# Optimization experiments

Measured on AMD Instinct MI355X. Metric: run time of the kernel, lower is better.

Reference implementation:

```python
import jax, jax.numpy as jnp
import numpy as np

EMBED_DIM = 768
NUM_HEADS = 12
HEAD_DIM = EMBED_DIM // NUM_HEADS
SCALE = HEAD_DIM ** -0.5


def setup_inputs() -> dict:
    key = jax.random.key(0)
    k_x, k_wqkv, k_bqkv, k_wp, k_bp = jax.random.split(key, 5)
    B, N, D = 16, 1024, EMBED_DIM
    x = jax.random.normal(k_x, (B, N, D), dtype=jnp.float32)
    # nn.Linear default init: U(-1/sqrt(fan_in), 1/sqrt(fan_in))
    bound = 1.0 / np.sqrt(D)
    W_qkv = jax.random.uniform(k_wqkv, (D, 3 * D), minval=-bound, maxval=bound, dtype=jnp.float32)
    b_qkv = jax.random.uniform(k_bqkv, (3 * D,), minval=-bound, maxval=bound, dtype=jnp.float32)
    W_proj = jax.random.uniform(k_wp, (D, D), minval=-bound, maxval=bound, dtype=jnp.float32)
    b_proj = jax.random.uniform(k_bp, (D,), minval=-bound, maxval=bound, dtype=jnp.float32)
    return {"x": x, "W_qkv": W_qkv, "b_qkv": b_qkv, "W_proj": W_proj, "b_proj": b_proj}


def reference(x, W_qkv, b_qkv, W_proj, b_proj):
    B, N, D = x.shape
    H, Hd = NUM_HEADS, HEAD_DIM
    qkv = x @ W_qkv + b_qkv                      # [B, N, 3D]
    qkv = qkv.reshape(B, N, 3, H, Hd)
    qkv = jnp.transpose(qkv, (2, 0, 3, 1, 4))    # [3, B, H, N, Hd]
    q, k, v = qkv[0], qkv[1], qkv[2]
    attn = jnp.einsum('bhnd,bhmd->bhnm', q, k) * SCALE  # [B, H, N, N]
    attn = jax.nn.softmax(attn, axis=-1)
    out = jnp.einsum('bhnm,bhmd->bhnd', attn, v)        # [B, H, N, Hd]
    out = jnp.transpose(out, (0, 2, 1, 3)).reshape(B, N, D)
    return out @ W_proj + b_proj
```

## Files before the change

### kernel.cpp

```cpp
#include <hip/hip_runtime.h>
#include <math.h>

typedef _Float16 f16;
typedef _Float16 f16x8 __attribute__((ext_vector_type(8)));
typedef _Float16 f16x4 __attribute__((ext_vector_type(4)));
typedef float    f32x4 __attribute__((ext_vector_type(4)));

#define AS1 __attribute__((address_space(1)))
#define AS3 __attribute__((address_space(3)))

__device__ __forceinline__ void gload16(const void* g, void* l) {
    __builtin_amdgcn_global_load_lds((const AS1 void*)g, (AS3 void*)l, 16, 0, 0);
}

__global__ __launch_bounds__(256) void cast_x_k(const float* __restrict__ in,
                                                f16* __restrict__ out, int n8)
{
    int i = blockIdx.x * 256 + threadIdx.x;
    const int stride = gridDim.x * 256;
    const float4* in4 = (const float4*)in;
    f16x8* o8 = (f16x8*)out;
    for (; i < n8; i += stride) {
        float4 a = in4[2 * i], b = in4[2 * i + 1];
        f16x8 o = {(f16)a.x, (f16)a.y, (f16)a.z, (f16)a.w,
                   (f16)b.x, (f16)b.y, (f16)b.z, (f16)b.w};
        o8[i] = o;
    }
}

__global__ __launch_bounds__(256) void castT_k(const float* __restrict__ W,
                                               f16* __restrict__ WT, int K, int N)
{
    __shared__ float tile[32][33];
    const int k0 = blockIdx.y * 32, n0 = blockIdx.x * 32;
    const int t = threadIdx.x;
    const int r = t >> 3, cq = t & 7;
    float4 v = *(const float4*)&W[(size_t)(k0 + r) * N + n0 + cq * 4];
    tile[r][cq * 4 + 0] = v.x; tile[r][cq * 4 + 1] = v.y;
    tile[r][cq * 4 + 2] = v.z; tile[r][cq * 4 + 3] = v.w;
    __syncthreads();
    f16x4 pk = {(f16)tile[cq * 4 + 0][r], (f16)tile[cq * 4 + 1][r],
                (f16)tile[cq * 4 + 2][r], (f16)tile[cq * 4 + 3][r]};
    *(f16x4*)&WT[(size_t)(n0 + r) * K + k0 + cq * 4] = pk;
}

__global__ __launch_bounds__(256) void vtrans_k(const f16* __restrict__ V,
                                                f16* __restrict__ VT)
{
    __shared__ __align__(16) f16 tile[64][72];
    const int bh = blockIdx.y, tt = blockIdx.x;
    const int t = threadIdx.x;
    const size_t base = (size_t)bh * 1024 * 64;
    {
        int tok = t >> 2, d0 = (t & 3) * 16;
        const f16* src = V + base + (size_t)(tt * 64 + tok) * 64 + d0;
        *(f16x8*)&tile[tok][d0]     = *(const f16x8*)src;
        *(f16x8*)&tile[tok][d0 + 8] = *(const f16x8*)(src + 8);
    }
    __syncthreads();
    {
        int d = t >> 2, ck = t & 3;
        f16 tmp[16];
#pragma unroll
        for (int j = 0; j < 16; ++j) tmp[j] = tile[ck * 16 + j][d];
        f16* dst = VT + base + (size_t)d * 1024 + tt * 64 + ck * 16;
        *(f16x8*)dst       = *(f16x8*)&tmp[0];
        *(f16x8*)(dst + 8) = *(f16x8*)&tmp[8];
    }
}

#define GEMM_MAIN(APTR, BTPTR)                                                   \
    __shared__ __align__(16) f16 As[128 * 64];                                   \
    __shared__ __align__(16) f16 Bs[128 * 64];                                   \
    const int t = threadIdx.x, lid = t & 63, wid = t >> 6;                       \
    const int wr = wid >> 1, wc = wid & 1;                                       \
    const int bm = blockIdx.y, bn = blockIdx.x;                                  \
    f32x4 acc[4][4] = {};                                                        \
    const int srow8 = lid >> 3;                                                  \
    const int sc = (lid & 7) ^ srow8;                                            \
    const f16* aG = (APTR) + (size_t)(bm * 128 + wid * 32 + srow8) * 768 + sc * 8;\
    const f16* bG = (BTPTR) + (size_t)(bn * 128 + wid * 32 + srow8) * 768 + sc * 8;\
    f16* ldsA = As + wid * 32 * 64;                                              \
    f16* ldsB = Bs + wid * 32 * 64;                                              \
    for (int k0 = 0; k0 < 768; k0 += 64) {                                       \
        __syncthreads();                                                         \
        _Pragma("unroll")                                                        \
        for (int c = 0; c < 4; ++c) {                                            \
            gload16(aG + c * 8 * 768 + k0, ldsA + c * 8 * 64);                   \
            gload16(bG + c * 8 * 768 + k0, ldsB + c * 8 * 64);                   \
        }                                                                        \
        __syncthreads();                                                         \
        _Pragma("unroll")                                                        \
        for (int kh = 0; kh < 2; ++kh) {                                         \
            f16x8 af[4], bf[4];                                                  \
            _Pragma("unroll")                                                    \
            for (int m = 0; m < 4; ++m) {                                        \
                int row = wr * 64 + m * 16 + (lid & 15);                         \
                int slot = (kh * 4 + (lid >> 4)) ^ (row & 7);                    \
                af[m] = *(const f16x8*)&As[row * 64 + slot * 8];                 \
                int col = wc * 64 + m * 16 + (lid & 15);                         \
                int slotb = (kh * 4 + (lid >> 4)) ^ (col & 7);                   \
                bf[m] = *(const f16x8*)&Bs[col * 64 + slotb * 8];                \
            }                                                                    \
            _Pragma("unroll")                                                    \
            for (int m = 0; m < 4; ++m)                                          \
                _Pragma("unroll")                                                \
                for (int n = 0; n < 4; ++n)                                      \
                    acc[m][n] = __builtin_amdgcn_mfma_f32_16x16x32_f16(          \
                        af[m], bf[n], acc[m][n], 0, 0, 0);                       \
        }                                                                        \
    }

__global__ __launch_bounds__(256)
void qkv_gemm16(const f16* __restrict__ A, const f16* __restrict__ BT,
                const float* __restrict__ bias,
                f16* __restrict__ qws, f16* __restrict__ kws, f16* __restrict__ vws)
{
    GEMM_MAIN(A, BT)
    const int g = lid >> 4, cl = lid & 15;
#pragma unroll
    for (int m = 0; m < 4; ++m) {
        int rbase = bm * 128 + wr * 64 + m * 16 + g * 4;
#pragma unroll
        for (int n = 0; n < 4; ++n) {
            int cg = bn * 128 + wc * 64 + n * 16 + cl;
            float bb = bias[cg];
            int which = cg / 768;
            int rem = cg - which * 768;
            int h = rem >> 6, d = rem & 63;
            f16* dst = (which == 0) ? qws : (which == 1) ? kws : vws;
            float scl = (which == 0) ? 0.125f : 1.0f;
#pragma unroll
            for (int r = 0; r < 4; ++r) {
                int row = rbase + r;
                int b = row >> 10, tok = row & 1023;
                dst[((size_t)(b * 12 + h) * 1024 + tok) * 64 + d] =
                    (f16)((acc[m][n][r] + bb) * scl);
            }
        }
    }
}

__global__ __launch_bounds__(256)
void proj_gemm16(const f16* __restrict__ A, const f16* __restrict__ BT,
                 const float* __restrict__ bias, float* __restrict__ C)
{
    GEMM_MAIN(A, BT)
    const int g = lid >> 4, cl = lid & 15;
#pragma unroll
    for (int m = 0; m < 4; ++m) {
        int rbase = bm * 128 + wr * 64 + m * 16 + g * 4;
#pragma unroll
        for (int n = 0; n < 4; ++n) {
            int cg = bn * 128 + wc * 64 + n * 16 + cl;
            float bb = bias[cg];
#pragma unroll
            for (int r = 0; r < 4; ++r)
                C[(size_t)(rbase + r) * 768 + cg] = acc[m][n][r] + bb;
        }
    }
}

__global__ __launch_bounds__(256)
void attn16(const f16* __restrict__ Q, const f16* __restrict__ K,
            const f16* __restrict__ VT, f16* __restrict__ AO)
{
    __shared__ __align__(16) f16 kbuf[2][64 * 64];
    __shared__ __align__(16) f16 vbuf[2][64 * 64];
    __shared__ __align__(16) f16 plds[4][16 * 64];

    const int t = threadIdx.x, lid = t & 63, wid = t >> 6;
    const int phys = blockIdx.y * gridDim.x + blockIdx.x;
    const int logical = (phys & 7) * 384 + (phys >> 3);
    const int bh = logical >> 4, qt = logical & 15;

    const int g = lid >> 4, c = lid & 15;
    const size_t hb = (size_t)bh * (1024 * 64);
    const int q0 = qt * 64 + wid * 16;

    const f16* qrow = Q + hb + (size_t)(q0 + c) * 64;
    const f16x8 qf0 = *(const f16x8*)(qrow + g * 8);
    const f16x8 qf1 = *(const f16x8*)(qrow + 32 + g * 8);

    const int srow   = wid * 16 + (lid >> 3);
    const int schunk = ((lid & 7) ^ (lid >> 3)) * 8;

#define ATTN_STAGE(BUF, KT)                                                      \
    {                                                                            \
        const f16* kb_ = K + hb + (size_t)((KT) * 64) * 64;                      \
        const f16* vb_ = VT + hb + (KT) * 64;                                    \
        _Pragma("unroll")                                                        \
        for (int c2 = 0; c2 < 2; ++c2) {                                         \
            gload16(kb_ + (size_t)(srow + c2 * 8) * 64 + schunk,                 \
                    &kbuf[BUF][wid * 1024 + c2 * 512]);                          \
            gload16(vb_ + (size_t)(srow + c2 * 8) * 1024 + schunk,               \
                    &vbuf[BUF][wid * 1024 + c2 * 512]);                          \
        }                                                                        \
    }

    f32x4 o[4] = {};
    float mrun = -INFINITY, lrun = 0.f;
    f16* myp = &plds[wid][0];

    ATTN_STAGE(0, 0)
    __syncthreads();

    int cur = 0;
    for (int kt = 0; kt < 16; ++kt) {
        if (kt < 15) ATTN_STAGE(cur ^ 1, kt + 1)

        const f16* kcur = &kbuf[cur][0];
        const f16* vcur = &vbuf[cur][0];
        const int sw = c & 7;

        f32x4 s[4] = {};
#pragma unroll
        for (int m = 0; m < 4; ++m) {
            const int row = m * 16 + c;
            f16x8 k0f = *(const f16x8*)&kcur[row * 64 + ((g) ^ sw) * 8];
            f16x8 k1f = *(const f16x8*)&kcur[row * 64 + ((4 + g) ^ sw) * 8];
            s[m] = __builtin_amdgcn_mfma_f32_16x16x32_f16(k0f, qf0, s[m], 0, 0, 0);
            s[m] = __builtin_amdgcn_mfma_f32_16x16x32_f16(k1f, qf1, s[m], 0, 0, 0);
        }
        float tmax = s[0][0];
#pragma unroll
        for (int m = 0; m < 4; ++m)
#pragma unroll
            for (int r = 0; r < 4; ++r) tmax = fmaxf(tmax, s[m][r]);
        tmax = fmaxf(tmax, __shfl_xor(tmax, 16));
        tmax = fmaxf(tmax, __shfl_xor(tmax, 32));
        float mnew = fmaxf(mrun, tmax);
        float al = __expf(mrun - mnew);
        float ps = 0.f;
        float pe[4][4];
#pragma unroll
        for (int m = 0; m < 4; ++m)
#pragma unroll
            for (int r = 0; r < 4; ++r) {
                float p = __expf(s[m][r] - mnew);
                pe[m][r] = p; ps += p;
            }
        ps += __shfl_xor(ps, 16);
        ps += __shfl_xor(ps, 32);
        lrun = lrun * al + ps;
        mrun = mnew;
#pragma unroll
        for (int m = 0; m < 4; ++m) {
            f16x4 pk = {(f16)pe[m][0], (f16)pe[m][1], (f16)pe[m][2], (f16)pe[m][3]};
            int slot = (2 * m + (g >> 1)) ^ sw;
            *(f16x4*)&myp[c * 64 + slot * 8 + (g & 1) * 4] = pk;
        }
        float al4[4];
#pragma unroll
        for (int r = 0; r < 4; ++r) al4[r] = __shfl(al, g * 4 + r);
#pragma unroll
        for (int n = 0; n < 4; ++n) {
            o[n][0] *= al4[0]; o[n][1] *= al4[1];
            o[n][2] *= al4[2]; o[n][3] *= al4[3];
        }
        f16x8 pa[2];
#pragma unroll
        for (int kh = 0; kh < 2; ++kh) {
            int slot = (kh * 4 + g) ^ sw;
            pa[kh] = *(const f16x8*)&myp[c * 64 + slot * 8];
        }
#pragma unroll
        for (int kh = 0; kh < 2; ++kh)
#pragma unroll
            for (int n = 0; n < 4; ++n) {
                const int row = n * 16 + c;
                f16x8 vf = *(const f16x8*)&vcur[row * 64 + ((kh * 4 + g) ^ sw) * 8];
                o[n] = __builtin_amdgcn_mfma_f32_16x16x32_f16(pa[kh], vf, o[n], 0, 0, 0);
            }

        __syncthreads();
        cur ^= 1;
    }

    float il = 1.0f / lrun;
    float il4[4];
#pragma unroll
    for (int r = 0; r < 4; ++r) il4[r] = __shfl(il, g * 4 + r);
    const int b = bh / 12, h = bh - b * 12;
#pragma unroll
    for (int n = 0; n < 4; ++n)
#pragma unroll
        for (int r = 0; r < 4; ++r) {
            int tok = q0 + g * 4 + r;
            AO[(size_t)(b * 1024 + tok) * 768 + h * 64 + n * 16 + c] =
                (f16)(o[n][r] * il4[r]);
        }
}


extern "C" void kernel_launch(void* const* d_in, const int* in_sizes, int n_in,
                              void* d_out, int out_size, void* d_ws, size_t ws_size,
                              hipStream_t stream)
{
    const float* x      = (const float*)d_in[0];
    const float* W_qkv  = (const float*)d_in[1];
    const float* b_qkv  = (const float*)d_in[2];
    const float* W_proj = (const float*)d_in[3];
    const float* b_proj = (const float*)d_in[4];
    float* out = (float*)d_out;

    const size_t per = (size_t)16 * 1024 * 768;
    f16* x16    = (f16*)d_ws;
    f16* wqkvT  = x16 + per;
    f16* wprojT = wqkvT + (size_t)768 * 2304;
    f16* qws    = wprojT + (size_t)768 * 768;
    f16* kws    = qws + per;
    f16* vws    = kws + per;
    f16* vt     = vws + per;
    f16* aws    = vt + per;

    cast_x_k<<<3072, 256, 0, stream>>>(x, x16, (int)(per / 8));
    castT_k<<<dim3(2304 / 32, 768 / 32), 256, 0, stream>>>(W_qkv, wqkvT, 768, 2304);
    castT_k<<<dim3(768 / 32, 768 / 32), 256, 0, stream>>>(W_proj, wprojT, 768, 768);
    qkv_gemm16<<<dim3(18, 128), 256, 0, stream>>>(x16, wqkvT, b_qkv, qws, kws, vws);
    vtrans_k<<<dim3(16, 192), 256, 0, stream>>>(vws, vt);
    attn16<<<dim3(16, 192), 256, 0, stream>>>(qws, kws, vt, aws);
    proj_gemm16<<<dim3(6, 128), 256, 0, stream>>>(aws, wprojT, b_proj, out);
}
```

Before: 341.9 us.

## Pipeline GEMMs with 4-stage LDS ring, fuse V transpose, add lazy softmax rescale

The two GEMMs now use 256x256 tiles with 512 threads, a 4-deep global-to-LDS prefetch ring in 32-wide K slices, XCD-aware block remapping and setprio around the MFMA blocks. The QKV epilogue writes V already transposed, which removes the separate vtrans kernel. Attention folds log2(e) into the Q scale so it can use exp2. It also skips rescaling the output accumulator when the running max grows by no more than a threshold. The trade-offs are higher register and LDS pressure in the GEMMs and a risk of f16 overflow in P if the threshold logic is wrong.

```diff
diff --git a/kernel.cpp b/kernel.cpp
--- a/kernel.cpp
+++ b/kernel.cpp
@@ -8,6 +8,8 @@
 
 #define AS1 __attribute__((address_space(1)))
 #define AS3 __attribute__((address_space(3)))
+
+#define QSCALE 0.1803368800f
 
 __device__ __forceinline__ void gload16(const void* g, void* l) {
     __builtin_amdgcn_global_load_lds((const AS1 void*)g, (AS3 void*)l, 16, 0, 0);
@@ -44,115 +46,111 @@
     *(f16x4*)&WT[(size_t)(n0 + r) * K + k0 + cq * 4] = pk;
 }
 
-__global__ __launch_bounds__(256) void vtrans_k(const f16* __restrict__ V,
-                                                f16* __restrict__ VT)
-{
-    __shared__ __align__(16) f16 tile[64][72];
-    const int bh = blockIdx.y, tt = blockIdx.x;
-    const int t = threadIdx.x;
-    const size_t base = (size_t)bh * 1024 * 64;
-    {
-        int tok = t >> 2, d0 = (t & 3) * 16;
-        const f16* src = V + base + (size_t)(tt * 64 + tok) * 64 + d0;
-        *(f16x8*)&tile[tok][d0]     = *(const f16x8*)src;
-        *(f16x8*)&tile[tok][d0 + 8] = *(const f16x8*)(src + 8);
-    }
-    __syncthreads();
-    {
-        int d = t >> 2, ck = t & 3;
-        f16 tmp[16];
-#pragma unroll
-        for (int j = 0; j < 16; ++j) tmp[j] = tile[ck * 16 + j][d];
-        f16* dst = VT + base + (size_t)d * 1024 + tt * 64 + ck * 16;
-        *(f16x8*)dst       = *(f16x8*)&tmp[0];
-        *(f16x8*)(dst + 8) = *(f16x8*)&tmp[8];
-    }
-}
-
-#define GEMM_MAIN(APTR, BTPTR)                                                   \
-    __shared__ __align__(16) f16 As[128 * 64];                                   \
-    __shared__ __align__(16) f16 Bs[128 * 64];                                   \
+#define GEMM_PIPE(APTR, BTPTR, NBN, PERX)                                        \
+    __shared__ __align__(16) f16 As[4][256 * 32];                                \
+    __shared__ __align__(16) f16 Bs[4][256 * 32];                                \
     const int t = threadIdx.x, lid = t & 63, wid = t >> 6;                       \
-    const int wr = wid >> 1, wc = wid & 1;                                       \
-    const int bm = blockIdx.y, bn = blockIdx.x;                                  \
-    f32x4 acc[4][4] = {};                                                        \
-    const int srow8 = lid >> 3;                                                  \
-    const int sc = (lid & 7) ^ srow8;                                            \
-    const f16* aG = (APTR) + (size_t)(bm * 128 + wid * 32 + srow8) * 768 + sc * 8;\
-    const f16* bG = (BTPTR) + (size_t)(bn * 128 + wid * 32 + srow8) * 768 + sc * 8;\
-    f16* ldsA = As + wid * 32 * 64;                                              \
-    f16* ldsB = Bs + wid * 32 * 64;                                              \
-    for (int k0 = 0; k0 < 768; k0 += 64) {                                       \
-        __syncthreads();                                                         \
-        _Pragma("unroll")                                                        \
-        for (int c = 0; c < 4; ++c) {                                            \
-            gload16(aG + c * 8 * 768 + k0, ldsA + c * 8 * 64);                   \
-            gload16(bG + c * 8 * 768 + k0, ldsB + c * 8 * 64);                   \
+    const int wr = wid >> 2, wc = wid & 3;                                       \
+    const int g = lid >> 4, cl = lid & 15;                                       \
+    const int flat = blockIdx.x;                                                 \
+    const int logical = (flat & 7) * (PERX) + (flat >> 3);                       \
+    const int bm = logical / (NBN), bn = logical % (NBN);                        \
+    f32x4 acc[8][4] = {};                                                        \
+    const f16* aG[2]; const f16* bG[2]; int ldsoff[2];                           \
+    _Pragma("unroll")                                                            \
+    for (int i = 0; i < 2; ++i) {                                                \
+        int c_lin = wid * 128 + i * 64 + lid;                                    \
+        int row = c_lin >> 2, ch = c_lin & 3;                                    \
+        int sch = ch ^ (row & 3);                                                \
+        aG[i] = (APTR) + (size_t)(bm * 256 + row) * 768 + sch * 8;               \
+        bG[i] = (BTPTR) + (size_t)(bn * 256 + row) * 768 + sch * 8;              \
+        ldsoff[i] = (wid * 128 + i * 64) * 8;                                    \
+    }                                                                            \
+    _Pragma("unroll")                                                            \
+    for (int p = 0; p < 3; ++p) {                                                \
+        _Pragma("unroll")                                                        \
+        for (int i = 0; i < 2; ++i) {                                            \
+            gload16(aG[i] + p * 32, &As[p][ldsoff[i]]);                          \
+            gload16(bG[i] + p * 32, &Bs[p][ldsoff[i]]);                          \
         }                                                                        \
-        __syncthreads();                                                         \
-        _Pragma("unroll")                                                        \
-        for (int kh = 0; kh < 2; ++kh) {                                         \
-            f16x8 af[4], bf[4];                                                  \
+    }                                                                            \
+    for (int kt = 0; kt < 24; ++kt) {                                            \
+        int tn = kt + 3; if (tn >= 24) tn -= 24;    \
+        _Pragma("unroll")                                                        \
+        for (int i = 0; i < 2; ++i) {                                            \
+            gload16(aG[i] + tn * 32, &As[tn & 3][ldsoff[i]]);                    \
+            gload16(bG[i] + tn * 32, &Bs[tn & 3][ldsoff[i]]);                    \
+        }                                                                        \
+        asm volatile("s_waitcnt vmcnt(12)" ::: "memory");                        \
+        __builtin_amdgcn_s_barrier();                                            \
+        const f16* As_ = &As[kt & 3][0];                                         \
+        const f16* Bs_ = &Bs[kt & 3][0];                                         \
+        const int slotx = (g ^ (cl & 3)) * 8;                                    \
+        f16x8 af[8], bf[4];                                                      \
+        _Pragma("unroll")                                                        \
+        for (int m = 0; m < 8; ++m)                                              \
+            af[m] = *(const f16x8*)&As_[(wr * 128 + m * 16 + cl) * 32 + slotx];  \
+        _Pragma("unroll")                                                        \
+        for (int n = 0; n < 4; ++n)                                              \
+            bf[n] = *(const f16x8*)&Bs_[(wc * 64 + n * 16 + cl) * 32 + slotx];   \
+        __builtin_amdgcn_s_setprio(1);                                           \
+        _Pragma("unroll")                                                        \
+        for (int m = 0; m < 8; ++m)                                              \
             _Pragma("unroll")                                                    \
-            for (int m = 0; m < 4; ++m) {                                        \
-                int row = wr * 64 + m * 16 + (lid & 15);                         \
-                int slot = (kh * 4 + (lid >> 4)) ^ (row & 7);                    \
-                af[m] = *(const f16x8*)&As[row * 64 + slot * 8];                 \
-                int col = wc * 64 + m * 16 + (lid & 15);                         \
-                int slotb = (kh * 4 + (lid >> 4)) ^ (col & 7);                   \
-                bf[m] = *(const f16x8*)&Bs[col * 64 + slotb * 8];                \
-            }                                                                    \
-            _Pragma("unroll")                                                    \
-            for (int m = 0; m < 4; ++m)                                          \
-                _Pragma("unroll")                                                \
-                for (int n = 0; n < 4; ++n)                                      \
-                    acc[m][n] = __builtin_amdgcn_mfma_f32_16x16x32_f16(          \
-                        af[m], bf[n], acc[m][n], 0, 0, 0);                       \
-        }                                                                        \
-    }
-
-__global__ __launch_bounds__(256)
+            for (int n = 0; n < 4; ++n)                                          \
+                acc[m][n] = __builtin_amdgcn_mfma_f32_16x16x32_f16(              \
+                    af[m], bf[n], acc[m][n], 0, 0, 0);                           \
+        __builtin_amdgcn_s_setprio(0);                                           \
+        __builtin_amdgcn_s_barrier();                                            \
+    }
+
+__global__ __launch_bounds__(512, 2)
 void qkv_gemm16(const f16* __restrict__ A, const f16* __restrict__ BT,
                 const float* __restrict__ bias,
-                f16* __restrict__ qws, f16* __restrict__ kws, f16* __restrict__ vws)
-{
-    GEMM_MAIN(A, BT)
-    const int g = lid >> 4, cl = lid & 15;
-#pragma unroll
-    for (int m = 0; m < 4; ++m) {
-        int rbase = bm * 128 + wr * 64 + m * 16 + g * 4;
+                f16* __restrict__ qws, f16* __restrict__ kws, f16* __restrict__ vt)
+{
+    GEMM_PIPE(A, BT, 9, 72)
+#pragma unroll
+    for (int m = 0; m < 8; ++m) {
+        int rbase = bm * 256 + wr * 128 + m * 16 + g * 4;
 #pragma unroll
         for (int n = 0; n < 4; ++n) {
-            int cg = bn * 128 + wc * 64 + n * 16 + cl;
+            int cg = bn * 256 + wc * 64 + n * 16 + cl;
             float bb = bias[cg];
             int which = cg / 768;
             int rem = cg - which * 768;
             int h = rem >> 6, d = rem & 63;
-            f16* dst = (which == 0) ? qws : (which == 1) ? kws : vws;
-            float scl = (which == 0) ? 0.125f : 1.0f;
-#pragma unroll
-            for (int r = 0; r < 4; ++r) {
-                int row = rbase + r;
-                int b = row >> 10, tok = row & 1023;
-                dst[((size_t)(b * 12 + h) * 1024 + tok) * 64 + d] =
-                    (f16)((acc[m][n][r] + bb) * scl);
+            if (which == 2) {
+                int b = rbase >> 10, tok = rbase & 1023;
+                f16x4 pk = {(f16)(acc[m][n][0] + bb), (f16)(acc[m][n][1] + bb),
+                            (f16)(acc[m][n][2] + bb), (f16)(acc[m][n][3] + bb)};
+                *(f16x4*)&vt[((size_t)(b * 12 + h) * 64 + d) * 1024 + tok] = pk;
+            } else {
+                f16* dst = which ? kws : qws;
+                float scl = which ? 1.0f : QSCALE;
+#pragma unroll
+                for (int r = 0; r < 4; ++r) {
+                    int row = rbase + r;
+                    int b = row >> 10, tok = row & 1023;
+                    dst[((size_t)(b * 12 + h) * 1024 + tok) * 64 + d] =
+                        (f16)((acc[m][n][r] + bb) * scl);
+                }
             }
         }
     }
 }
 
-__global__ __launch_bounds__(256)
+__global__ __launch_bounds__(512, 2)
 void proj_gemm16(const f16* __restrict__ A, const f16* __restrict__ BT,
                  const float* __restrict__ bias, float* __restrict__ C)
 {
-    GEMM_MAIN(A, BT)
-    const int g = lid >> 4, cl = lid & 15;
-#pragma unroll
-    for (int m = 0; m < 4; ++m) {
-        int rbase = bm * 128 + wr * 64 + m * 16 + g * 4;
+    GEMM_PIPE(A, BT, 3, 24)
+#pragma unroll
+    for (int m = 0; m < 8; ++m) {
+        int rbase = bm * 256 + wr * 128 + m * 16 + g * 4;
 #pragma unroll
         for (int n = 0; n < 4; ++n) {
-            int cg = bn * 128 + wc * 64 + n * 16 + cl;
+            int cg = bn * 256 + wc * 64 + n * 16 + cl;
             float bb = bias[cg];
 #pragma unroll
             for (int r = 0; r < 4; ++r)
@@ -214,6 +212,7 @@
         const int sw = c & 7;
 
         f32x4 s[4] = {};
+        __builtin_amdgcn_s_setprio(1);
 #pragma unroll
         for (int m = 0; m < 4; ++m) {
             const int row = m * 16 + c;
@@ -222,48 +221,61 @@
             s[m] = __builtin_amdgcn_mfma_f32_16x16x32_f16(k0f, qf0, s[m], 0, 0, 0);
             s[m] = __builtin_amdgcn_mfma_f32_16x16x32_f16(k1f, qf1, s[m], 0, 0, 0);
         }
-        float tmax = s[0][0];
-#pragma unroll
-        for (int m = 0; m < 4; ++m)
-#pragma unroll
-            for (int r = 0; r < 4; ++r) tmax = fmaxf(tmax, s[m][r]);
+        __builtin_amdgcn_s_setprio(0);
+
+        float a0 = fmaxf(fmaxf(s[0][0], s[0][1]), fmaxf(s[0][2], s[0][3]));
+        float a1 = fmaxf(fmaxf(s[1][0], s[1][1]), fmaxf(s[1][2], s[1][3]));
+        float a2 = fmaxf(fmaxf(s[2][0], s[2][1]), fmaxf(s[2][2], s[2][3]));
+        float a3 = fmaxf(fmaxf(s[3][0], s[3][1]), fmaxf(s[3][2], s[3][3]));
+        float tmax = fmaxf(fmaxf(a0, a1), fmaxf(a2, a3));
         tmax = fmaxf(tmax, __shfl_xor(tmax, 16));
         tmax = fmaxf(tmax, __shfl_xor(tmax, 32));
+
+        bool keep = __all(tmax - mrun <= 8.0f);
         float mnew = fmaxf(mrun, tmax);
-        float al = __expf(mrun - mnew);
+        float mref = keep ? mrun : mnew;
+
         float ps = 0.f;
         float pe[4][4];
 #pragma unroll
         for (int m = 0; m < 4; ++m)
 #pragma unroll
             for (int r = 0; r < 4; ++r) {
-                float p = __expf(s[m][r] - mnew);
+                float p = __builtin_exp2f(s[m][r] - mref);
                 pe[m][r] = p; ps += p;
             }
         ps += __shfl_xor(ps, 16);
         ps += __shfl_xor(ps, 32);
-        lrun = lrun * al + ps;
-        mrun = mnew;
+
+        if (keep) {
+            lrun += ps;
+        } else {
+            float al = __builtin_exp2f(mrun - mnew);
+            float al4[4];
+#pragma unroll
+            for (int r = 0; r < 4; ++r) al4[r] = __shfl(al, g * 4 + r);
+#pragma unroll
+            for (int n = 0; n < 4; ++n) {
+                o[n][0] *= al4[0]; o[n][1] *= al4[1];
+                o[n][2] *= al4[2]; o[n][3] *= al4[3];
+            }
+            lrun = lrun * al + ps;
+            mrun = mnew;
+        }
+
 #pragma unroll
         for (int m = 0; m < 4; ++m) {
             f16x4 pk = {(f16)pe[m][0], (f16)pe[m][1], (f16)pe[m][2], (f16)pe[m][3]};
             int slot = (2 * m + (g >> 1)) ^ sw;
             *(f16x4*)&myp[c * 64 + slot * 8 + (g & 1) * 4] = pk;
         }
-        float al4[4];
-#pragma unroll
-        for (int r = 0; r < 4; ++r) al4[r] = __shfl(al, g * 4 + r);
-#pragma unroll
-        for (int n = 0; n < 4; ++n) {
-            o[n][0] *= al4[0]; o[n][1] *= al4[1];
-            o[n][2] *= al4[2]; o[n][3] *= al4[3];
-        }
         f16x8 pa[2];
 #pragma unroll
         for (int kh = 0; kh < 2; ++kh) {
             int slot = (kh * 4 + g) ^ sw;
             pa[kh] = *(const f16x8*)&myp[c * 64 + slot * 8];
         }
+        __builtin_amdgcn_s_setprio(1);
 #pragma unroll
         for (int kh = 0; kh < 2; ++kh)
 #pragma unroll
@@ -272,6 +284,7 @@
                 f16x8 vf = *(const f16x8*)&vcur[row * 64 + ((kh * 4 + g) ^ sw) * 8];
                 o[n] = __builtin_amdgcn_mfma_f32_16x16x32_f16(pa[kh], vf, o[n], 0, 0, 0);
             }
+        __builtin_amdgcn_s_setprio(0);
 
         __syncthreads();
         cur ^= 1;
@@ -310,15 +323,13 @@
     f16* wprojT = wqkvT + (size_t)768 * 2304;
     f16* qws    = wprojT + (size_t)768 * 768;
     f16* kws    = qws + per;
-    f16* vws    = kws + per;
-    f16* vt     = vws + per;
+    f16* vt     = kws + per;
     f16* aws    = vt + per;
 
     cast_x_k<<<3072, 256, 0, stream>>>(x, x16, (int)(per / 8));
     castT_k<<<dim3(2304 / 32, 768 / 32), 256, 0, stream>>>(W_qkv, wqkvT, 768, 2304);
     castT_k<<<dim3(768 / 32, 768 / 32), 256, 0, stream>>>(W_proj, wprojT, 768, 768);
-    qkv_gemm16<<<dim3(18, 128), 256, 0, stream>>>(x16, wqkvT, b_qkv, qws, kws, vws);
-    vtrans_k<<<dim3(16, 192), 256, 0, stream>>>(vws, vt);
+    qkv_gemm16<<<576, 512, 0, stream>>>(x16, wqkvT, b_qkv, qws, kws, vt);
     attn16<<<dim3(16, 192), 256, 0, stream>>>(qws, kws, vt, aws);
-    proj_gemm16<<<dim3(6, 128), 256, 0, stream>>>(aws, wprojT, b_proj, out);
-}
+    proj_gemm16<<<192, 512, 0, stream>>>(aws, wprojT, b_proj, out);
+}
```

After: 369.3 us. 1.08x slower.
